# Kernel optimization log

Hardware: AMD Instinct MI355X
Metric: run time of the kernel (lower is better)

Reference implementation:

```python
import jax, jax.numpy as jnp
import numpy as np

B, N, D = 8, 2048, 512
S = 4096  # max_swaps


def setup_inputs() -> dict:
    key = jax.random.key(0)
    ks = jax.random.split(key, 5)
    h = jax.random.normal(ks[0], (B, N, D), dtype=jnp.float32)
    indices = jax.random.randint(ks[1], (B, S, 4), 0, N, dtype=jnp.int64)
    # MLP params (Linear stores weight as (out,in) in torch; we keep (in,out) and matmul)
    W1 = jax.random.normal(ks[2], (4 * D, D), dtype=jnp.float32) * (1.0 / np.sqrt(4 * D))
    b1 = jnp.zeros((D,), dtype=jnp.float32)
    W2 = jax.random.normal(ks[3], (D, D // 2), dtype=jnp.float32) * (1.0 / np.sqrt(D))
    b2 = jnp.zeros((D // 2,), dtype=jnp.float32)
    W3 = jax.random.normal(ks[4], (D // 2, 1), dtype=jnp.float32) * (1.0 / np.sqrt(D // 2))
    b3 = jnp.zeros((1,), dtype=jnp.float32)
    return {"h": h, "indices": indices, "W1": W1, "b1": b1, "W2": W2, "b2": b2, "W3": W3, "b3": b3}


def reference(h, indices, W1, b1, W2, b2, W3, b3):
    # h: (B, N, D); indices: (B, S, 4) node ids per swap
    swap_emb = jnp.take_along_axis(h[:, None, :, :], indices[..., None].astype(jnp.int32),
                                   axis=2)  # broadcast-gather -> (B, S, 4, D)
    # equivalently: h[batch_idx, indices]; implemented as per-batch gather
    swap_emb = jax.vmap(lambda hb, ib: hb[ib])(h, indices)  # (B, S, 4, D)
    swap_feats = swap_emb.reshape(h.shape[0], indices.shape[1], -1)  # (B, S, 4D)
    x = jax.nn.gelu(swap_feats @ W1 + b1, approximate=False)
    x = jax.nn.gelu(x @ W2 + b2, approximate=False)
    scores = (x @ W3 + b3)[..., 0]  # (B, S)
    rates = jax.nn.softplus(scores)
    return rates
```

## Files before the change

kernel.cpp:

```cpp
#include <hip/hip_runtime.h>
#include <math.h>

#define BATCH 8
#define NNODES 2048
#define DDIM 512
#define SWAPS 4096
#define M_TOTAL (BATCH * SWAPS)
#define KD DDIM
#define K2 DDIM
#define N2 (DDIM / 2)

typedef __attribute__((ext_vector_type(8))) __bf16 bf16x8;
typedef __attribute__((ext_vector_type(4))) float f32x4;
typedef __attribute__((ext_vector_type(8))) unsigned short us8;
typedef unsigned short ushort_t;

__device__ __forceinline__ float gelu_fast(float x) {
    const float u = 0.7978845608028654f * x * fmaf(0.044715f * x, x, 1.0f);
    const float e = __expf(-2.0f * fabsf(u));
    float t = (1.0f - e) / (1.0f + e);
    t = copysignf(t, u);
    return 0.5f * x * (1.0f + t);
}
__device__ __forceinline__ float softplus_f(float x) {
    return fmaxf(x, 0.0f) + log1pf(expf(-fabsf(x)));
}
__device__ __forceinline__ unsigned short f2bf(float f) {
    unsigned int u = __builtin_bit_cast(unsigned int, f);
    u += 0x7FFFu + ((u >> 16) & 1u);
    return (unsigned short)(u >> 16);
}
__device__ __forceinline__ float bf2f(unsigned short s) {
    return __builtin_bit_cast(float, (unsigned int)s << 16);
}
__device__ __forceinline__ void glds16(const void* g, void* l) {
    __builtin_amdgcn_global_load_lds(
        (const __attribute__((address_space(1))) void*)g,
        (__attribute__((address_space(3))) void*)l, 16, 0, 0);
}

__global__ __launch_bounds__(256) void convert_kernel(
    const float* __restrict__ h, const float* __restrict__ W1,
    const float* __restrict__ W2, ushort_t* __restrict__ h_bf,
    ushort_t* __restrict__ W1pt, ushort_t* __restrict__ W2f)
{
    const int bid = blockIdx.x;
    const int tid = threadIdx.x;
    if (bid < 4096) {
        const size_t i = ((size_t)bid * 256 + tid) * 8;
        float4 v0 = *(const float4*)(h + i);
        float4 v1 = *(const float4*)(h + i + 4);
        us8 o;
        o[0] = f2bf(v0.x); o[1] = f2bf(v0.y); o[2] = f2bf(v0.z); o[3] = f2bf(v0.w);
        o[4] = f2bf(v1.x); o[5] = f2bf(v1.y); o[6] = f2bf(v1.z); o[7] = f2bf(v1.w);
        *(us8*)(h_bf + i) = o;
    } else if (bid < 4096 + 256) {
        __shared__ ushort_t sT[64][72];
        const int tb = bid - 4096;
        const int kt = tb >> 3, nt = tb & 7;
        const int kl = tid >> 4;
        const int n4 = (tid & 15) * 4;
        #pragma unroll
        for (int p = 0; p < 4; ++p) {
            const int k_local = p * 16 + kl;
            float4 v = *(const float4*)(W1 + (size_t)(kt * 64 + k_local) * 512
                                        + nt * 64 + n4);
            sT[n4 + 0][k_local] = f2bf(v.x);
            sT[n4 + 1][k_local] = f2bf(v.y);
            sT[n4 + 2][k_local] = f2bf(v.z);
            sT[n4 + 3][k_local] = f2bf(v.w);
        }
        __syncthreads();
        const int n_local = tid >> 2, ch = tid & 3;
        const int j = (kt >> 3) * 512 + nt * 64 + n_local;
        const int d0 = (kt & 7) * 64 + ch * 16;
        us8 o0, o1;
        #pragma unroll
        for (int e = 0; e < 8; ++e) { o0[e] = sT[n_local][ch * 16 + e];
                                      o1[e] = sT[n_local][ch * 16 + 8 + e]; }
        *(us8*)(W1pt + (size_t)j * KD + d0)     = o0;
        *(us8*)(W1pt + (size_t)j * KD + d0 + 8) = o1;
    } else {
        size_t e = ((size_t)(bid - 4352) * 256 + tid) * 4;
        const int k = (int)(e >> 8), n = (int)(e & 255);
        const int kc = k >> 5, quad = (k >> 3) & 3, pos = k & 7;
        const size_t base = (size_t)kc * 8192 + quad * 8 + pos;
        float4 v = *(const float4*)(W2 + e);
        W2f[base + (size_t)(n + 0) * 32] = f2bf(v.x);
        W2f[base + (size_t)(n + 1) * 32] = f2bf(v.y);
        W2f[base + (size_t)(n + 2) * 32] = f2bf(v.z);
        W2f[base + (size_t)(n + 3) * 32] = f2bf(v.w);
    }
}

__global__ __launch_bounds__(256, 4) void gemm1_dense(
    const ushort_t* __restrict__ h_bf, const ushort_t* __restrict__ W1pt,
    ushort_t* __restrict__ P2)
{
    __shared__ __align__(16) char smem[32768];

    const int tid = threadIdx.x;
    const int w = tid >> 6, lane = tid & 63;
    const int quad = lane >> 4, l16 = lane & 15;
    const int wr = w >> 1, wc = w & 1;

    const int bid = blockIdx.x;
    const int xcd = bid & 7;
    const int r = bid >> 3;
    const int m0 = xcd * NNODES + (r & 15) * 128;
    const int n0 = (r >> 4) * 128;

    const int row0 = tid >> 2, sub = tid & 3;
    const int cg = (sub - (row0 >> 1)) & 3;
    const ushort_t* bA0 = h_bf + (size_t)(m0 + row0) * KD + cg * 8;
    const ushort_t* bA1 = h_bf + (size_t)(m0 + row0 + 64) * KD + cg * 8;
    const ushort_t* bB0 = W1pt + (size_t)(n0 + row0) * KD + cg * 8;
    const ushort_t* bB1 = W1pt + (size_t)(n0 + row0 + 64) * KD + cg * 8;

    int pa[4], pb[4];
    #pragma unroll
    for (int i = 0; i < 4; ++i) {
        const int rA = wr * 64 + i * 16 + l16;
        const int rB = wc * 64 + i * 16 + l16;
        pa[i] = rA * 64 + (((quad + (rA >> 1)) & 3) * 16);
        pb[i] = 8192 + rB * 64 + (((quad + (rB >> 1)) & 3) * 16);
    }

    f32x4 acc[4][4] = {};

    auto stage = [&](int kt, int half) {
        const int oo = kt * 32;
        char* base = smem + half * 16384;
        glds16(bA0 + oo, base + w * 1024);
        glds16(bA1 + oo, base + 4096 + w * 1024);
        glds16(bB0 + oo, base + 8192 + w * 1024);
        glds16(bB1 + oo, base + 12288 + w * 1024);
    };
    auto compute = [&](int half) {
        const char* base = smem + half * 16384;
        bf16x8 af[4], bfr[4];
        #pragma unroll
        for (int i = 0; i < 4; ++i) {
            af[i]  = *(const bf16x8*)(base + pa[i]);
            bfr[i] = *(const bf16x8*)(base + pb[i]);
        }
        #pragma unroll
        for (int i = 0; i < 4; ++i)
            #pragma unroll
            for (int jj = 0; jj < 4; ++jj)
                acc[i][jj] = __builtin_amdgcn_mfma_f32_16x16x32_bf16(
                    af[i], bfr[jj], acc[i][jj], 0, 0, 0);
    };

    for (int kt = 0; kt < 16; kt += 2) {
        stage(kt, 0);
        stage(kt + 1, 1);
        __syncthreads();
        compute(0);
        compute(1);
        __syncthreads();
    }

    #pragma unroll
    for (int jj = 0; jj < 4; ++jj) {
        const int j = n0 + wc * 64 + jj * 16 + l16;
        const int sg = j >> 9, nh = j & 511;
        const size_t base = ((size_t)(xcd * 2 + (nh >> 8)) * NNODES) * 1024
                          + (size_t)(sg << 8) + (nh & 255);
        #pragma unroll
        for (int i = 0; i < 4; ++i) {
            f32x4 v = acc[i][jj];
            #pragma unroll
            for (int rr = 0; rr < 4; ++rr) {
                const int node = (m0 + wr * 64 + i * 16 + quad * 4 + rr) & (NNODES - 1);
                P2[base + (size_t)node * 1024] = f2bf(v[rr]);
            }
        }
    }
}

__global__ __launch_bounds__(512) void fused_tail(
    const ushort_t* __restrict__ P2, const int* __restrict__ idx,
    const float* __restrict__ b1, const ushort_t* __restrict__ W2f,
    const float* __restrict__ b2, const float* __restrict__ W3,
    const float* __restrict__ b3, float* __restrict__ out)
{
    __shared__ __align__(16) char smem[66560];

    const int tid = threadIdx.x;
    const int w = tid >> 6, lane = tid & 63;
    const int quad = lane >> 4, l16 = lane & 15;

    const int bid = blockIdx.x;
    const int b = bid & 7;
    const int m0 = b * SWAPS + (bid >> 3) * 64;

    {
        const int row = tid >> 3;
        const int ws  = tid & 7;
        const int ap  = ws & 3;
        const int ncs = ws >> 2;
        const int acg = (ap - (row >> 1)) & 3;
        const int4 iv = *(const int4*)(idx + (size_t)(m0 + row) * 4);
        const ushort_t* Pr = P2 + (size_t)(b * 2 + ncs) * NNODES * 1024;
        const ushort_t* p0 = Pr + (size_t)iv.x * 1024 + 0 * 256;
        const ushort_t* p1 = Pr + (size_t)iv.y * 1024 + 1 * 256;
        const ushort_t* p2 = Pr + (size_t)iv.z * 1024 + 2 * 256;
        const ushort_t* p3 = Pr + (size_t)iv.w * 1024 + 3 * 256;
        #pragma unroll 4
        for (int it = 0; it < 8; ++it) {
            const int kc = ncs * 8 + it;
            const int pos0 = it * 32 + acg * 8;
            us8 v0 = *(const us8*)(p0 + pos0);
            us8 v1 = *(const us8*)(p1 + pos0);
            us8 v2 = *(const us8*)(p2 + pos0);
            us8 v3 = *(const us8*)(p3 + pos0);
            const float* bp = b1 + ncs * 256 + pos0;
            float4 ba = *(const float4*)bp;
            float4 bb = *(const float4*)(bp + 4);
            float s[8] = { ba.x, ba.y, ba.z, ba.w, bb.x, bb.y, bb.z, bb.w };
            #pragma unroll
            for (int e = 0; e < 8; ++e)
                s[e] += bf2f(v0[e]) + bf2f(v1[e]) + bf2f(v2[e]) + bf2f(v3[e]);
            us8 o;
            #pragma unroll
            for (int e = 0; e < 8; ++e) o[e] = f2bf(gelu_fast(s[e]));
            *(us8*)(smem + kc * 4096 + row * 64 + ap * 16) = o;
        }
    }
    __syncthreads();

    const int rg = w >> 2, cg = w & 3;
    int paRow[2];
    #pragma unroll
    for (int i = 0; i < 2; ++i) {
        const int rA = rg * 32 + i * 16 + l16;
        paRow[i] = rA * 64 + (((quad + (rA >> 1)) & 3) * 16);
    }
    const ushort_t* Bbase = W2f + (size_t)(cg * 64 + l16) * 32 + quad * 8;

    f32x4 acc[2][4] = {};

    #pragma unroll 2
    for (int kc = 0; kc < 16; ++kc) {
        bf16x8 af0 = *(const bf16x8*)(smem + kc * 4096 + paRow[0]);
        bf16x8 af1 = *(const bf16x8*)(smem + kc * 4096 + paRow[1]);
        #pragma unroll
        for (int jf = 0; jf < 4; ++jf) {
            bf16x8 bfr = *(const bf16x8*)(Bbase + (size_t)kc * 8192 + jf * 512);
            acc[0][jf] = __builtin_amdgcn_mfma_f32_16x16x32_bf16(af0, bfr, acc[0][jf], 0, 0, 0);
            acc[1][jf] = __builtin_amdgcn_mfma_f32_16x16x32_bf16(af1, bfr, acc[1][jf], 0, 0, 0);
        }
    }

    float part[2][4] = {};
    #pragma unroll
    for (int jf = 0; jf < 4; ++jf) {
        const int n = cg * 64 + jf * 16 + l16;
        const float w3 = W3[n];
        const float bb2 = b2[n];
        #pragma unroll
        for (int i = 0; i < 2; ++i) {
            f32x4 v = acc[i][jf];
            #pragma unroll
            for (int rr = 0; rr < 4; ++rr)
                part[i][rr] = fmaf(gelu_fast(v[rr] + bb2), w3, part[i][rr]);
        }
    }
    #pragma unroll
    for (int off = 1; off < 16; off <<= 1)
        #pragma unroll
        for (int i = 0; i < 2; ++i)
            #pragma unroll
            for (int rr = 0; rr < 4; ++rr)
                part[i][rr] += __shfl_xor(part[i][rr], off);

    float* red = (float*)(smem + 65536);
    if (l16 == 0) {
        #pragma unroll
        for (int i = 0; i < 2; ++i)
            #pragma unroll
            for (int rr = 0; rr < 4; ++rr)
                red[cg * 64 + rg * 32 + i * 16 + quad * 4 + rr] = part[i][rr];
    }
    __syncthreads();
    if (tid < 64) {
        const float v = red[tid] + red[64 + tid] + red[128 + tid] + red[192 + tid];
        out[m0 + tid] = softplus_f(v + b3[0]);
    }
}

extern "C" void kernel_launch(void* const* d_in, const int* in_sizes, int n_in,
                              void* d_out, int out_size, void* d_ws, size_t ws_size,
                              hipStream_t stream) {
    const float* h   = (const float*)d_in[0];
    const int*   idx = (const int*)d_in[1];
    const float* W1  = (const float*)d_in[2];
    const float* b1  = (const float*)d_in[3];
    const float* W2  = (const float*)d_in[4];
    const float* b2  = (const float*)d_in[5];
    const float* W3  = (const float*)d_in[6];
    const float* b3  = (const float*)d_in[7];
    float* out = (float*)d_out;

    char* ws = (char*)d_ws;
    ushort_t* P2    = (ushort_t*)ws;
    ushort_t* h_bf  = (ushort_t*)(ws + (64u << 20));
    ushort_t* W1pt  = (ushort_t*)(ws + (80u << 20));
    ushort_t* W2f   = (ushort_t*)(ws + (82u << 20));

    convert_kernel<<<4480, 256, 0, stream>>>(h, W1, W2, h_bf, W1pt, W2f);
    gemm1_dense<<<2048, 256, 0, stream>>>(h_bf, W1pt, P2);
    fused_tail<<<512, 512, 0, stream>>>(P2, idx, b1, W2f, b2, W3, b3, out);
}
```

Before: 166.4 us.

## Double-buffer fused tail to overlap gather/GELU with MFMA across two row tiles

Each fused_tail block now processes two 64-row tiles using two LDS buffers. The gather and first GELU for the second tile are interleaved with the second-layer MFMA of the first tile, so gather memory latency is hidden behind matrix work. The grid is halved and LDS use doubles, forcing one block per CU and reducing the number of resident waves available to hide latency.

```diff
diff --git a/kernel.cpp b/kernel.cpp
--- a/kernel.cpp
+++ b/kernel.cpp
@@ -179,13 +179,13 @@
     }
 }
 
-__global__ __launch_bounds__(512) void fused_tail(
+__global__ __launch_bounds__(512, 1) void fused_tail(
     const ushort_t* __restrict__ P2, const int* __restrict__ idx,
     const float* __restrict__ b1, const ushort_t* __restrict__ W2f,
     const float* __restrict__ b2, const float* __restrict__ W3,
     const float* __restrict__ b3, float* __restrict__ out)
 {
-    __shared__ __align__(16) char smem[66560];
+    __shared__ __align__(16) char smem[132096];
 
     const int tid = threadIdx.x;
     const int w = tid >> 6, lane = tid & 63;
@@ -193,101 +193,145 @@
 
     const int bid = blockIdx.x;
     const int b = bid & 7;
-    const int m0 = b * SWAPS + (bid >> 3) * 64;
+    const int m0 = b * SWAPS + (bid >> 3) * 128;
+
+    const int grow = tid >> 3;
+    const int gws  = tid & 7;
+    const int ap   = gws & 3;
+    const int ncs  = gws >> 2;
+    const int acg  = (ap - (grow >> 1)) & 3;
+    const ushort_t* PrB = P2 + (size_t)(b * 2 + ncs) * NNODES * 1024;
+
+    auto geluStore = [&](char* buf, int it, us8 v0, us8 v1, us8 v2, us8 v3) {
+        const int kc = ncs * 8 + it;
+        const int pos0 = it * 32 + acg * 8;
+        const float* bp = b1 + ncs * 256 + pos0;
+        float4 ba = *(const float4*)bp;
+        float4 bb = *(const float4*)(bp + 4);
+        float s[8] = { ba.x, ba.y, ba.z, ba.w, bb.x, bb.y, bb.z, bb.w };
+        #pragma unroll
+        for (int e = 0; e < 8; ++e)
+            s[e] += bf2f(v0[e]) + bf2f(v1[e]) + bf2f(v2[e]) + bf2f(v3[e]);
+        us8 o;
+        #pragma unroll
+        for (int e = 0; e < 8; ++e) o[e] = f2bf(gelu_fast(s[e]));
+        *(us8*)(buf + kc * 4096 + grow * 64 + ap * 16) = o;
+    };
+
+    const int rg = w >> 2, cgw = w & 3;
+    int paRow[2];
+    #pragma unroll
+    for (int i = 0; i < 2; ++i) {
+        const int rA = rg * 32 + i * 16 + l16;
+        paRow[i] = rA * 64 + (((quad + (rA >> 1)) & 3) * 16);
+    }
+    const ushort_t* Bbase = W2f + (size_t)(cgw * 64 + l16) * 32 + quad * 8;
+
+    float* red = (float*)(smem + 131072);
+    auto head = [&](f32x4 (&A)[2][4], int mt, bool preBar) {
+        float part[2][4] = {};
+        #pragma unroll
+        for (int jf = 0; jf < 4; ++jf) {
+            const int n = cgw * 64 + jf * 16 + l16;
+            const float w3 = W3[n];
+            const float bb2 = b2[n];
+            #pragma unroll
+            for (int i = 0; i < 2; ++i) {
+                f32x4 v = A[i][jf];
+                #pragma unroll
+                for (int rr = 0; rr < 4; ++rr)
+                    part[i][rr] = fmaf(gelu_fast(v[rr] + bb2), w3, part[i][rr]);
+            }
+        }
+        #pragma unroll
+        for (int off = 1; off < 16; off <<= 1)
+            #pragma unroll
+            for (int i = 0; i < 2; ++i)
+                #pragma unroll
+                for (int rr = 0; rr < 4; ++rr)
+                    part[i][rr] += __shfl_xor(part[i][rr], off);
+        if (preBar) __syncthreads();
+        if (l16 == 0) {
+            #pragma unroll
+            for (int i = 0; i < 2; ++i)
+                #pragma unroll
+                for (int rr = 0; rr < 4; ++rr)
+                    red[cgw * 64 + rg * 32 + i * 16 + quad * 4 + rr] = part[i][rr];
+        }
+        __syncthreads();
+        if (tid < 64) {
+            const float v = red[tid] + red[64 + tid] + red[128 + tid] + red[192 + tid];
+            out[mt + tid] = softplus_f(v + b3[0]);
+        }
+    };
+
+    char* buf0 = smem;
+    char* buf1 = smem + 65536;
 
     {
-        const int row = tid >> 3;
-        const int ws  = tid & 7;
-        const int ap  = ws & 3;
-        const int ncs = ws >> 2;
-        const int acg = (ap - (row >> 1)) & 3;
-        const int4 iv = *(const int4*)(idx + (size_t)(m0 + row) * 4);
-        const ushort_t* Pr = P2 + (size_t)(b * 2 + ncs) * NNODES * 1024;
-        const ushort_t* p0 = Pr + (size_t)iv.x * 1024 + 0 * 256;
-        const ushort_t* p1 = Pr + (size_t)iv.y * 1024 + 1 * 256;
-        const ushort_t* p2 = Pr + (size_t)iv.z * 1024 + 2 * 256;
-        const ushort_t* p3 = Pr + (size_t)iv.w * 1024 + 3 * 256;
+        const int4 iv = *(const int4*)(idx + (size_t)(m0 + grow) * 4);
+        const ushort_t* p0 = PrB + (size_t)iv.x * 1024 + 0 * 256;
+        const ushort_t* p1 = PrB + (size_t)iv.y * 1024 + 1 * 256;
+        const ushort_t* p2 = PrB + (size_t)iv.z * 1024 + 2 * 256;
+        const ushort_t* p3 = PrB + (size_t)iv.w * 1024 + 3 * 256;
         #pragma unroll 4
         for (int it = 0; it < 8; ++it) {
-            const int kc = ncs * 8 + it;
             const int pos0 = it * 32 + acg * 8;
             us8 v0 = *(const us8*)(p0 + pos0);
             us8 v1 = *(const us8*)(p1 + pos0);
             us8 v2 = *(const us8*)(p2 + pos0);
             us8 v3 = *(const us8*)(p3 + pos0);
-            const float* bp = b1 + ncs * 256 + pos0;
-            float4 ba = *(const float4*)bp;
-            float4 bb = *(const float4*)(bp + 4);
-            float s[8] = { ba.x, ba.y, ba.z, ba.w, bb.x, bb.y, bb.z, bb.w };
-            #pragma unroll
-            for (int e = 0; e < 8; ++e)
-                s[e] += bf2f(v0[e]) + bf2f(v1[e]) + bf2f(v2[e]) + bf2f(v3[e]);
-            us8 o;
-            #pragma unroll
-            for (int e = 0; e < 8; ++e) o[e] = f2bf(gelu_fast(s[e]));
-            *(us8*)(smem + kc * 4096 + row * 64 + ap * 16) = o;
+            geluStore(buf0, it, v0, v1, v2, v3);
         }
     }
     __syncthreads();
 
-    const int rg = w >> 2, cg = w & 3;
-    int paRow[2];
-    #pragma unroll
-    for (int i = 0; i < 2; ++i) {
-        const int rA = rg * 32 + i * 16 + l16;
-        paRow[i] = rA * 64 + (((quad + (rA >> 1)) & 3) * 16);
-    }
-    const ushort_t* Bbase = W2f + (size_t)(cg * 64 + l16) * 32 + quad * 8;
-
-    f32x4 acc[2][4] = {};
-
+    f32x4 acc0[2][4] = {};
+    auto mfma2 = [&](const char* buf, int kc0, f32x4 (&A)[2][4]) {
+        #pragma unroll
+        for (int kc = kc0; kc < kc0 + 2; ++kc) {
+            bf16x8 af0 = *(const bf16x8*)(buf + kc * 4096 + paRow[0]);
+            bf16x8 af1 = *(const bf16x8*)(buf + kc * 4096 + paRow[1]);
+            #pragma unroll
+            for (int jf = 0; jf < 4; ++jf) {
+                bf16x8 bfr = *(const bf16x8*)(Bbase + (size_t)kc * 8192 + jf * 512);
+                A[0][jf] = __builtin_amdgcn_mfma_f32_16x16x32_bf16(af0, bfr, A[0][jf], 0, 0, 0);
+                A[1][jf] = __builtin_amdgcn_mfma_f32_16x16x32_bf16(af1, bfr, A[1][jf], 0, 0, 0);
+            }
+        }
+    };
+    {
+        const int4 iv = *(const int4*)(idx + (size_t)(m0 + 64 + grow) * 4);
+        const ushort_t* q0 = PrB + (size_t)iv.x * 1024 + 0 * 256;
+        const ushort_t* q1 = PrB + (size_t)iv.y * 1024 + 1 * 256;
+        const ushort_t* q2 = PrB + (size_t)iv.z * 1024 + 2 * 256;
+        const ushort_t* q3 = PrB + (size_t)iv.w * 1024 + 3 * 256;
+        auto loadC = [&](int it, us8& v0, us8& v1, us8& v2, us8& v3) {
+            const int pos0 = it * 32 + acg * 8;
+            v0 = *(const us8*)(q0 + pos0);
+            v1 = *(const us8*)(q1 + pos0);
+            v2 = *(const us8*)(q2 + pos0);
+            v3 = *(const us8*)(q3 + pos0);
+        };
+        us8 a0, a1, a2, a3, c0, c1, c2, c3;
+        loadC(0, a0, a1, a2, a3);
+        #pragma unroll
+        for (int it = 0; it < 8; it += 2) {
+            loadC(it + 1, c0, c1, c2, c3);
+            mfma2(buf0, it * 2, acc0);
+            geluStore(buf1, it, a0, a1, a2, a3);
+            if (it + 2 < 8) loadC(it + 2, a0, a1, a2, a3);
+            mfma2(buf0, it * 2 + 2, acc0);
+            geluStore(buf1, it + 1, c0, c1, c2, c3);
+        }
+    }
+
+    head(acc0, m0, false);
+
+    f32x4 acc1[2][4] = {};
     #pragma unroll 2
-    for (int kc = 0; kc < 16; ++kc) {
-        bf16x8 af0 = *(const bf16x8*)(smem + kc * 4096 + paRow[0]);
-        bf16x8 af1 = *(const bf16x8*)(smem + kc * 4096 + paRow[1]);
-        #pragma unroll
-        for (int jf = 0; jf < 4; ++jf) {
-            bf16x8 bfr = *(const bf16x8*)(Bbase + (size_t)kc * 8192 + jf * 512);
-            acc[0][jf] = __builtin_amdgcn_mfma_f32_16x16x32_bf16(af0, bfr, acc[0][jf], 0, 0, 0);
-            acc[1][jf] = __builtin_amdgcn_mfma_f32_16x16x32_bf16(af1, bfr, acc[1][jf], 0, 0, 0);
-        }
-    }
-
-    float part[2][4] = {};
-    #pragma unroll
-    for (int jf = 0; jf < 4; ++jf) {
-        const int n = cg * 64 + jf * 16 + l16;
-        const float w3 = W3[n];
-        const float bb2 = b2[n];
-        #pragma unroll
-        for (int i = 0; i < 2; ++i) {
-            f32x4 v = acc[i][jf];
-            #pragma unroll
-            for (int rr = 0; rr < 4; ++rr)
-                part[i][rr] = fmaf(gelu_fast(v[rr] + bb2), w3, part[i][rr]);
-        }
-    }
-    #pragma unroll
-    for (int off = 1; off < 16; off <<= 1)
-        #pragma unroll
-        for (int i = 0; i < 2; ++i)
-            #pragma unroll
-            for (int rr = 0; rr < 4; ++rr)
-                part[i][rr] += __shfl_xor(part[i][rr], off);
-
-    float* red = (float*)(smem + 65536);
-    if (l16 == 0) {
-        #pragma unroll
-        for (int i = 0; i < 2; ++i)
-            #pragma unroll
-            for (int rr = 0; rr < 4; ++rr)
-                red[cg * 64 + rg * 32 + i * 16 + quad * 4 + rr] = part[i][rr];
-    }
-    __syncthreads();
-    if (tid < 64) {
-        const float v = red[tid] + red[64 + tid] + red[128 + tid] + red[192 + tid];
-        out[m0 + tid] = softplus_f(v + b3[0]);
-    }
+    for (int kc = 0; kc < 16; kc += 2) mfma2(buf1, kc, acc1);
+    head(acc1, m0 + 64, true);
 }
 
 extern "C" void kernel_launch(void* const* d_in, const int* in_sizes, int n_in,
@@ -311,5 +355,5 @@
 
     convert_kernel<<<4480, 256, 0, stream>>>(h, W1, W2, h_bf, W1pt, W2f);
     gemm1_dense<<<2048, 256, 0, stream>>>(h_bf, W1pt, P2);
-    fused_tail<<<512, 512, 0, stream>>>(P2, idx, b1, W2f, b2, W3, b3, out);
-}
+    fused_tail<<<256, 512, 0, stream>>>(P2, idx, b1, W2f, b2, W3, b3, out);
+}
```

Result: no change. 169.6 us (+1.9%).
